# Kernel optimization log

Measured on AMD Instinct MI355X. Metric: run time of the kernel, lower is better.

## Reference

```python
import jax, jax.numpy as jnp
import numpy as np
import math

B, S, D_MODEL, N_HEAD, D_HEAD, D_FFN = 1, 2048, 1024, 16, 64, 4096
EPS = 1e-6


def setup_inputs() -> dict:
    key = jax.random.key(0)
    ks = jax.random.split(key, 10)
    scale = 0.02
    x = jax.random.normal(ks[0], (B, S, D_MODEL), dtype=jnp.float32)
    # RoPE frequencies: freqs_cis[s, i] = exp(1j * s * theta_i), theta_i = 10000^{-2i/d_head}
    half = D_HEAD // 2
    inv_freq = 1.0 / (10000.0 ** (jnp.arange(0, half, dtype=jnp.float32) * 2.0 / D_HEAD))
    angles = jnp.arange(S, dtype=jnp.float32)[:, None] * inv_freq[None, :]  # [S, half]
    freqs_cos = jnp.cos(angles)
    freqs_sin = jnp.sin(angles)
    wq = jax.random.normal(ks[1], (D_MODEL, N_HEAD * D_HEAD), dtype=jnp.float32) * scale
    wk = jax.random.normal(ks[2], (D_MODEL, N_HEAD * D_HEAD), dtype=jnp.float32) * scale
    wv = jax.random.normal(ks[3], (D_MODEL, N_HEAD * D_HEAD), dtype=jnp.float32) * scale
    wo = jax.random.normal(ks[4], (N_HEAD * D_HEAD, D_MODEL), dtype=jnp.float32) * scale
    w1 = jax.random.normal(ks[5], (D_MODEL, D_FFN), dtype=jnp.float32) * scale
    w2 = jax.random.normal(ks[6], (D_FFN, D_MODEL), dtype=jnp.float32) * scale
    w3 = jax.random.normal(ks[7], (D_MODEL, D_FFN), dtype=jnp.float32) * scale
    attn_norm_w = jnp.ones((D_MODEL,), dtype=jnp.float32)
    ffn_norm_w = jnp.ones((D_MODEL,), dtype=jnp.float32)
    return {"x": x, "freqs_cos": freqs_cos, "freqs_sin": freqs_sin,
            "wq": wq, "wk": wk, "wv": wv, "wo": wo,
            "w1": w1, "w2": w2, "w3": w3,
            "attn_norm_w": attn_norm_w, "ffn_norm_w": ffn_norm_w}


def _rmsnorm(x, w):
    xf = x.astype(jnp.float32)
    inv = jax.lax.rsqrt(jnp.mean(xf * xf, axis=-1, keepdims=True) + EPS)
    return (xf * inv).astype(x.dtype) * w


def _rope(t, cos, sin):
    # t: [B, S, H, D]; treat last dim as interleaved (even, odd) complex pairs
    b, s, h, d = t.shape
    tr = t.astype(jnp.float32).reshape(b, s, h, d // 2, 2)
    te, to = tr[..., 0], tr[..., 1]
    c = cos[None, :, None, :]
    sn = sin[None, :, None, :]
    out = jnp.stack([te * c - to * sn, te * sn + to * c], axis=-1)
    return out.reshape(b, s, h, d).astype(t.dtype)


def reference(x, freqs_cos, freqs_sin, wq, wk, wv, wo, w1, w2, w3, attn_norm_w, ffn_norm_w):
    bsz, seqlen, _ = x.shape
    # --- attention sub-block ---
    hin = _rmsnorm(x, attn_norm_w)
    q = (hin @ wq).reshape(bsz, seqlen, N_HEAD, D_HEAD)
    k = (hin @ wk).reshape(bsz, seqlen, N_HEAD, D_HEAD)
    v = (hin @ wv).reshape(bsz, seqlen, N_HEAD, D_HEAD)
    q = _rope(q, freqs_cos, freqs_sin)
    k = _rope(k, freqs_cos, freqs_sin)
    # [B, H, S, S] scores, softmax in fp32 (no causal mask in original)
    scores = jnp.einsum('bqhd,bkhd->bhqk', q, k) / math.sqrt(D_HEAD)
    probs = jax.nn.softmax(scores.astype(jnp.float32), axis=-1).astype(q.dtype)
    attn = jnp.einsum('bhqk,bkhd->bqhd', probs, v).reshape(bsz, seqlen, N_HEAD * D_HEAD)
    h = x + attn @ wo
    # --- SwiGLU FFN sub-block ---
    f = _rmsnorm(h, ffn_norm_w)
    ffn = (jax.nn.silu(f @ w1) * (f @ w3)) @ w2
    return h + ffn
```

## Files before the change

kernel.cpp:

```cpp
#include <hip/hip_runtime.h>
#include <stdint.h>
#include <stddef.h>

using bf16x8 = __attribute__((ext_vector_type(8))) __bf16;
using f32x4  = __attribute__((ext_vector_type(4))) float;

__device__ __forceinline__ float bf2f(unsigned short u) {
  union { unsigned int i; float f; } v; v.i = ((unsigned int)u) << 16; return v.f;
}
__device__ __forceinline__ unsigned short f2bf(float f) {
  union { float f; unsigned int i; } v; v.f = f;
  unsigned int r = v.i + 0x7fffu + ((v.i >> 16) & 1u);
  return (unsigned short)(r >> 16);
}
__device__ __forceinline__ unsigned short f2bf_trunc(float f) {
  union { float f; unsigned int i; } v; v.f = f;
  return (unsigned short)(v.i >> 16);
}
__device__ __forceinline__ void async16(const void* g, void* l) {
  __builtin_amdgcn_global_load_lds(
      (const __attribute__((address_space(1))) unsigned int*)g,
      (__attribute__((address_space(3))) unsigned int*)l, 16, 0, 0);
}

#define S_LEN 2048
#define DMODEL 1024
#define NHEAD 16
#define DHEAD 64
#define DFFN 4096

struct T4 {
  const float *s0, *s1, *s2, *s3;
  unsigned short *d0, *d1, *d2, *d3;
};
__global__ __launch_bounds__(256) void transpose4_k(T4 j) {
  const float* in = blockIdx.z == 0 ? j.s0 : blockIdx.z == 1 ? j.s1 : blockIdx.z == 2 ? j.s2 : j.s3;
  unsigned short* out = blockIdx.z == 0 ? j.d0 : blockIdx.z == 1 ? j.d1 : blockIdx.z == 2 ? j.d2 : j.d3;
  __shared__ unsigned short tile[32][33];
  const int tx = threadIdx.x & 31;
  const int ty = threadIdx.x >> 5;
  const int bc = blockIdx.x * 32;
  const int br = blockIdx.y * 32;
#pragma unroll
  for (int i = 0; i < 4; ++i)
    tile[ty + i * 8][tx] = f2bf(in[(size_t)(br + ty + i * 8) * 1024 + bc + tx]);
  __syncthreads();
#pragma unroll
  for (int i = 0; i < 4; ++i)
    out[(size_t)(bc + ty + i * 8) * 1024 + br + tx] = tile[tx][ty + i * 8];
}

__global__ __launch_bounds__(256) void transpose13_k(
    const float* __restrict__ w1, const float* __restrict__ w3,
    unsigned short* __restrict__ out) {
  const float* in = blockIdx.z ? w3 : w1;
  const int rb = blockIdx.z * 16;
  __shared__ unsigned short tile[32][33];
  const int tx = threadIdx.x & 31;
  const int ty = threadIdx.x >> 5;
  const int bc = blockIdx.x * 32;
  const int br = blockIdx.y * 32;
#pragma unroll
  for (int i = 0; i < 4; ++i)
    tile[ty + i * 8][tx] = f2bf(in[(size_t)(br + ty + i * 8) * 4096 + bc + tx]);
  __syncthreads();
#pragma unroll
  for (int i = 0; i < 4; ++i) {
    int c = bc + ty + i * 8;
    int dest = (c >> 4) * 32 + rb + (c & 15);
    out[(size_t)dest * 1024 + br + tx] = tile[tx][ty + i * 8];
  }
}

__global__ __launch_bounds__(256) void transpose_w2_k(
    const float* __restrict__ in, unsigned short* __restrict__ out) {
  __shared__ unsigned short tile[32][33];
  const int tx = threadIdx.x & 31;
  const int ty = threadIdx.x >> 5;
  const int bc = blockIdx.x * 32;
  const int br = blockIdx.y * 32;
#pragma unroll
  for (int i = 0; i < 4; ++i)
    tile[ty + i * 8][tx] = f2bf(in[(size_t)(br + ty + i * 8) * 1024 + bc + tx]);
  __syncthreads();
#pragma unroll
  for (int i = 0; i < 4; ++i)
    out[(size_t)(bc + ty + i * 8) * 4096 + br + tx] = tile[tx][ty + i * 8];
}

__global__ __launch_bounds__(256) void vtrans_k(
    const unsigned short* __restrict__ QKV, unsigned short* __restrict__ VtG) {
  __shared__ unsigned short tile[32][33];
  const int tx = threadIdx.x & 31;
  const int ty = threadIdx.x >> 5;
  const int bc = blockIdx.x * 32;
  const int br = blockIdx.y * 32;
#pragma unroll
  for (int i = 0; i < 4; ++i)
    tile[ty + i * 8][tx] = QKV[(size_t)(br + ty + i * 8) * 3072 + 2048 + bc + tx];
  __syncthreads();
#pragma unroll
  for (int i = 0; i < 4; ++i)
    VtG[(size_t)(bc + ty + i * 8) * 2048 + br + tx] = tile[tx][ty + i * 8];
}

__global__ __launch_bounds__(256) void rmsnorm_k(
    const float* __restrict__ X, const float* __restrict__ W,
    unsigned short* __restrict__ Y) {
  const int row = blockIdx.x;
  const int t = threadIdx.x;
  const int lane = t & 63, w = t >> 6;
  const float* x = X + (size_t)row * DMODEL;
  float xs[4];
  float s = 0.f;
#pragma unroll
  for (int i = 0; i < 4; ++i) {
    xs[i] = x[t * 4 + i];
    s += xs[i] * xs[i];
  }
#pragma unroll
  for (int m = 1; m < 64; m <<= 1) s += __shfl_xor(s, m, 64);
  __shared__ float red[4];
  if (lane == 0) red[w] = s;
  __syncthreads();
  float tot = red[0] + red[1] + red[2] + red[3];
  float inv = rsqrtf(tot * (1.0f / DMODEL) + 1e-6f);
#pragma unroll
  for (int i = 0; i < 4; ++i)
    Y[(size_t)row * DMODEL + t * 4 + i] = f2bf(xs[i] * inv * W[t * 4 + i]);
}

template <int MODE>
__global__ __launch_bounds__(256) void gemm_bt(
    const unsigned short* __restrict__ A, int lda,
    const unsigned short* __restrict__ BT,
    void* __restrict__ Cout,
    int K, int N) {
  __shared__ unsigned short As[128 * 32];
  __shared__ unsigned short Bs[128 * 32];
  const int t = threadIdx.x;
  const int lane = t & 63;
  const int w = t >> 6;
  const int qr = (w >> 1) * 64, qc = (w & 1) * 64;
  const int row16 = lane & 15, quad = lane >> 4;
  const int m0 = blockIdx.y * 128, n0 = blockIdx.x * 128;

  f32x4 acc[4][4] = {};

  for (int k0 = 0; k0 < K; k0 += 32) {
    __syncthreads();
#pragma unroll
    for (int p = 0; p < 2; ++p) {
      int off = p * 2048 + t * 8;
      int r = off >> 5, c = off & 31;
      async16(A + (size_t)(m0 + r) * lda + (k0 + c), &As[off]);
      async16(BT + (size_t)(n0 + r) * K + (k0 + c), &Bs[off]);
    }
    __syncthreads();
    bf16x8 a[4], b[4];
#pragma unroll
    for (int i = 0; i < 4; ++i) {
      a[i] = *(const bf16x8*)&As[(qr + i * 16 + row16) * 32 + quad * 8];
      b[i] = *(const bf16x8*)&Bs[(qc + i * 16 + row16) * 32 + quad * 8];
    }
#pragma unroll
    for (int i = 0; i < 4; ++i)
#pragma unroll
      for (int j = 0; j < 4; ++j)
        acc[i][j] = __builtin_amdgcn_mfma_f32_16x16x32_bf16(a[i], b[j], acc[i][j], 0, 0, 0);
  }

  if constexpr (MODE == 2) {
    unsigned short* C = (unsigned short*)Cout;
    const int ld = N >> 1;
#pragma unroll
    for (int i = 0; i < 4; ++i)
#pragma unroll
      for (int jp = 0; jp < 4; jp += 2)
#pragma unroll
        for (int reg = 0; reg < 4; ++reg) {
          int rr = m0 + qr + i * 16 + quad * 4 + reg;
          int cc = (n0 >> 1) + (qc >> 1) + (jp >> 1) * 16 + row16;
          float a1 = acc[i][jp][reg];
          float a3 = acc[i][jp + 1][reg];
          float f = a1 / (1.f + __expf(-a1)) * a3;
          C[(size_t)rr * ld + cc] = f2bf(f);
        }
  } else {
    unsigned short* C = (unsigned short*)Cout;
#pragma unroll
    for (int i = 0; i < 4; ++i)
#pragma unroll
      for (int j = 0; j < 4; ++j)
#pragma unroll
        for (int reg = 0; reg < 4; ++reg) {
          int rr = m0 + qr + i * 16 + quad * 4 + reg;
          int cc = n0 + qc + j * 16 + row16;
          C[(size_t)rr * N + cc] = f2bf(acc[i][j][reg]);
        }
  }
}

struct PtrPair { float* p0; float* p1; };

__global__ __launch_bounds__(256) void gemm_bt_sk(
    const unsigned short* __restrict__ A, int lda,
    const unsigned short* __restrict__ BT,
    PtrPair parts, int Kc, int Ktot, int N) {
  __shared__ unsigned short As[64 * 32];
  __shared__ unsigned short Bs[128 * 32];
  const int t = threadIdx.x;
  const int lane = t & 63;
  const int w = t >> 6;
  const int qr = (w >> 1) * 32, qc = (w & 1) * 64;
  const int row16 = lane & 15, quad = lane >> 4;
  const int m0 = blockIdx.y * 64, n0 = blockIdx.x * 128;
  const int kb = blockIdx.z * Kc;

  f32x4 acc[2][4] = {};

  for (int k0 = 0; k0 < Kc; k0 += 32) {
    __syncthreads();
    {
      int off = t * 8;
      int r = off >> 5, c = off & 31;
      async16(A + (size_t)(m0 + r) * lda + (kb + k0 + c), &As[off]);
    }
#pragma unroll
    for (int p = 0; p < 2; ++p) {
      int off = p * 2048 + t * 8;
      int r = off >> 5, c = off & 31;
      async16(BT + (size_t)(n0 + r) * Ktot + (kb + k0 + c), &Bs[off]);
    }
    __syncthreads();
    bf16x8 a[2], b[4];
#pragma unroll
    for (int i = 0; i < 2; ++i)
      a[i] = *(const bf16x8*)&As[(qr + i * 16 + row16) * 32 + quad * 8];
#pragma unroll
    for (int j = 0; j < 4; ++j)
      b[j] = *(const bf16x8*)&Bs[(qc + j * 16 + row16) * 32 + quad * 8];
#pragma unroll
    for (int i = 0; i < 2; ++i)
#pragma unroll
      for (int j = 0; j < 4; ++j)
        acc[i][j] = __builtin_amdgcn_mfma_f32_16x16x32_bf16(a[i], b[j], acc[i][j], 0, 0, 0);
  }

  float* C = blockIdx.z ? parts.p1 : parts.p0;
#pragma unroll
  for (int i = 0; i < 2; ++i)
#pragma unroll
    for (int j = 0; j < 4; ++j)
#pragma unroll
      for (int reg = 0; reg < 4; ++reg) {
        int rr = m0 + qr + i * 16 + quad * 4 + reg;
        int cc = n0 + qc + j * 16 + row16;
        C[(size_t)rr * N + cc] = acc[i][j][reg];
      }
}

__global__ __launch_bounds__(256) void reduce2_k(
    const float4* __restrict__ P0, const float4* __restrict__ P1,
    const float4* __restrict__ R, float4* __restrict__ Out, int nvec) {
  int i = blockIdx.x * 256 + threadIdx.x;
  if (i >= nvec) return;
  float4 a = P0[i], b = P1[i], r = R[i];
  float4 o;
  o.x = a.x + b.x + r.x;
  o.y = a.y + b.y + r.y;
  o.z = a.z + b.z + r.z;
  o.w = a.w + b.w + r.w;
  Out[i] = o;
}

__global__ __launch_bounds__(256) void rope_k(
    unsigned short* __restrict__ QKV,
    const float* __restrict__ cosp,
    const float* __restrict__ sinp) {
  int idx = blockIdx.x * 256 + threadIdx.x;
  int s = idx >> 9;
  int rem = idx & 511;
  int h = rem >> 5;
  int i = rem & 31;
  float c = cosp[s * 32 + i];
  float sn = sinp[s * 32 + i];
  size_t off = (size_t)s * 3072 + h * 64 + 2 * i;
  {
    float e = bf2f(QKV[off]), o = bf2f(QKV[off + 1]);
    QKV[off] = f2bf(e * c - o * sn);
    QKV[off + 1] = f2bf(e * sn + o * c);
  }
  {
    float e = bf2f(QKV[off + 1024]), o = bf2f(QKV[off + 1025]);
    QKV[off + 1024] = f2bf((e * c - o * sn) * 0.125f);
    QKV[off + 1025] = f2bf((e * sn + o * c) * 0.125f);
  }
}

#define VPAD 132
__device__ __forceinline__ int swz(int row, int col) { return col ^ ((row & 7) * 8); }

__global__ __launch_bounds__(256) void attn_k(
    const unsigned short* __restrict__ QKV,
    const unsigned short* __restrict__ VtG,
    float* __restrict__ O0, float* __restrict__ O1,
    float* __restrict__ L) {
  const int h = blockIdx.y;
  const int qb = blockIdx.x;
  const int z = blockIdx.z;
  const int t = threadIdx.x;
  const int lane = t & 63;
  const int w = t >> 6;
  const int row16 = lane & 15, quad = lane >> 4;
  const int q0 = qb * 64 + w * 16;
  const int kbase = z * 1024;

  __shared__ unsigned short Ks[128 * 64];
  __shared__ unsigned short Vt[64 * 128];
  __shared__ unsigned short Ps[4][16 * VPAD];

  const unsigned short* Qp = QKV;
  const unsigned short* Kp = QKV + 1024;
  const unsigned short* Vg = VtG + (size_t)h * 64 * 2048;

  bf16x8 aq[2];
#pragma unroll
  for (int kk = 0; kk < 2; ++kk)
    aq[kk] = *(const bf16x8*)(Qp + (size_t)(q0 + row16) * 3072 + h * 64 + kk * 32 + quad * 8);

  f32x4 o[4] = {};
  float l_r[4] = {0.f, 0.f, 0.f, 0.f};

  bf16x8 kreg[4], vreg[4];
#pragma unroll
  for (int p = 0; p < 4; ++p) {
    int off = p * 2048 + t * 8;
    int r = off >> 6, c = off & 63;
    kreg[p] = *(const bf16x8*)(Kp + (size_t)(kbase + r) * 3072 + h * 64 + c);
    int d = off >> 7, key = off & 127;
    vreg[p] = *(const bf16x8*)(Vg + (size_t)d * 2048 + kbase + key);
  }

  for (int kb = kbase; kb < kbase + 1024; kb += 128) {
    __syncthreads();
#pragma unroll
    for (int p = 0; p < 4; ++p) {
      int off = p * 2048 + t * 8;
      int r = off >> 6, c = off & 63;
      *(bf16x8*)&Ks[r * 64 + swz(r, c)] = kreg[p];
      int d = off >> 7, key = off & 127;
      *(bf16x8*)&Vt[d * 128 + swz(d, key)] = vreg[p];
    }
    __syncthreads();
    if (kb + 128 < kbase + 1024) {
      int kb2 = kb + 128;
#pragma unroll
      for (int p = 0; p < 4; ++p) {
        int off = p * 2048 + t * 8;
        int r = off >> 6, c = off & 63;
        kreg[p] = *(const bf16x8*)(Kp + (size_t)(kb2 + r) * 3072 + h * 64 + c);
        int d = off >> 7, key = off & 127;
        vreg[p] = *(const bf16x8*)(Vg + (size_t)d * 2048 + kb2 + key);
      }
    }

    f32x4 sc[8];
#pragma unroll
    for (int tj = 0; tj < 8; ++tj) {
      int kr = tj * 16 + row16;
      bf16x8 b0 = *(const bf16x8*)&Ks[kr * 64 + swz(kr, quad * 8)];
      bf16x8 b1 = *(const bf16x8*)&Ks[kr * 64 + swz(kr, 32 + quad * 8)];
      f32x4 z4 = {};
      z4 = __builtin_amdgcn_mfma_f32_16x16x32_bf16(aq[0], b0, z4, 0, 0, 0);
      z4 = __builtin_amdgcn_mfma_f32_16x16x32_bf16(aq[1], b1, z4, 0, 0, 0);
      sc[tj] = z4;
    }

#pragma unroll
    for (int reg = 0; reg < 4; ++reg) {
      float ssum = 0.f;
#pragma unroll
      for (int tj = 0; tj < 8; ++tj) {
        float p = __expf(sc[tj][reg]);
        sc[tj][reg] = p;
        ssum += p;
      }
#pragma unroll
      for (int m = 1; m < 16; m <<= 1) ssum += __shfl_xor(ssum, m, 16);
      l_r[reg] += ssum;
    }

#pragma unroll
    for (int tj = 0; tj < 8; ++tj)
#pragma unroll
      for (int reg = 0; reg < 4; ++reg)
        Ps[w][(quad * 4 + reg) * VPAD + tj * 16 + row16] = f2bf_trunc(sc[tj][reg]);

    bf16x8 ap[4];
#pragma unroll
    for (int kk = 0; kk < 4; ++kk)
      ap[kk] = *(const bf16x8*)&Ps[w][row16 * VPAD + kk * 32 + quad * 8];
#pragma unroll
    for (int dt = 0; dt < 4; ++dt) {
      int dr = dt * 16 + row16;
#pragma unroll
      for (int kk = 0; kk < 4; ++kk) {
        bf16x8 bv = *(const bf16x8*)&Vt[dr * 128 + swz(dr, kk * 32 + quad * 8)];
        o[dt] = __builtin_amdgcn_mfma_f32_16x16x32_bf16(ap[kk], bv, o[dt], 0, 0, 0);
      }
    }
  }

  float* Op = z ? O1 : O0;
#pragma unroll
  for (int dt = 0; dt < 4; ++dt)
#pragma unroll
    for (int reg = 0; reg < 4; ++reg)
      Op[(size_t)(q0 + quad * 4 + reg) * DMODEL + h * 64 + dt * 16 + row16] = o[dt][reg];
  if (row16 == 0)
#pragma unroll
    for (int reg = 0; reg < 4; ++reg)
      L[(size_t)(h * 2 + z) * S_LEN + q0 + quad * 4 + reg] = l_r[reg];
}

__global__ __launch_bounds__(256) void attn_combine_k(
    const float4* __restrict__ O0, const float4* __restrict__ O1,
    const float* __restrict__ L, unsigned short* __restrict__ Attn) {
  int i = blockIdx.x * 256 + threadIdx.x;
  int e0 = i * 4;
  int s = e0 >> 10;
  int c = e0 & 1023;
  int h = c >> 6;
  float la = L[(size_t)(h * 2) * S_LEN + s];
  float lb = L[(size_t)(h * 2 + 1) * S_LEN + s];
  float inv = 1.f / (la + lb);
  float4 a = O0[i], b = O1[i];
  ushort4 r;
  r.x = f2bf((a.x + b.x) * inv);
  r.y = f2bf((a.y + b.y) * inv);
  r.z = f2bf((a.z + b.z) * inv);
  r.w = f2bf((a.w + b.w) * inv);
  *(ushort4*)(Attn + e0) = r;
}

extern "C" void kernel_launch(void* const* d_in, const int* in_sizes, int n_in,
                              void* d_out, int out_size, void* d_ws, size_t ws_size,
                              hipStream_t stream) {
  (void)in_sizes; (void)n_in; (void)out_size; (void)ws_size;
  const float* x    = (const float*)d_in[0];
  const float* fcos = (const float*)d_in[1];
  const float* fsin = (const float*)d_in[2];
  const float* wq   = (const float*)d_in[3];
  const float* wk   = (const float*)d_in[4];
  const float* wv   = (const float*)d_in[5];
  const float* wo   = (const float*)d_in[6];
  const float* w1   = (const float*)d_in[7];
  const float* w2   = (const float*)d_in[8];
  const float* w3   = (const float*)d_in[9];
  const float* anw  = (const float*)d_in[10];
  const float* fnw  = (const float*)d_in[11];
  float* out = (float*)d_out;
  char* ws = (char*)d_ws;

  unsigned short* WqkvT = (unsigned short*)(ws + 0);
  unsigned short* VtG   = (unsigned short*)(ws + 0);
  float*          Lbuf  = (float*)(ws + 4194304);
  unsigned short* WoT   = (unsigned short*)(ws + 6291456);
  unsigned short* QKV   = (unsigned short*)(ws + 8388608);
  unsigned short* Attn  = (unsigned short*)(ws + 20971520);
  float* Oa             = (float*)(ws + 25165824);
  float* Ob             = (float*)(ws + 37748736);
  float* P0a            = (float*)(ws + 8388608);
  float* P1a            = (float*)(ws + 25165824);
  unsigned short* F     = (unsigned short*)(ws + 0);
  float* P0b            = (float*)(ws + 16777216);
  float* P1b            = (float*)(ws + 25165824);
  unsigned short* Hin   = (unsigned short*)(ws + 33554432);
  float*          Hres  = (float*)        (ws + 37748736);
  unsigned short* W13I  = (unsigned short*)(ws + 46137344);
  unsigned short* W2T   = (unsigned short*)(ws + 62914560);

  transpose4_k<<<dim3(32, 32, 4), 256, 0, stream>>>(
      T4{wq, wk, wv, wo, WqkvT, WqkvT + 1048576, WqkvT + 2097152, WoT});
  transpose13_k<<<dim3(128, 32, 2), 256, 0, stream>>>(w1, w3, W13I);
  transpose_w2_k<<<dim3(32, 128), 256, 0, stream>>>(w2, W2T);

  rmsnorm_k<<<2048, 256, 0, stream>>>(x, anw, Hin);
  gemm_bt<0><<<dim3(24, 16), 256, 0, stream>>>(Hin, 1024, WqkvT, QKV, 1024, 3072);
  rope_k<<<4096, 256, 0, stream>>>(QKV, fcos, fsin);
  vtrans_k<<<dim3(32, 64), 256, 0, stream>>>(QKV, VtG);
  attn_k<<<dim3(32, 16, 2), 256, 0, stream>>>(QKV, VtG, Oa, Ob, Lbuf);
  attn_combine_k<<<2048, 256, 0, stream>>>((const float4*)Oa, (const float4*)Ob, Lbuf, Attn);
  gemm_bt_sk<<<dim3(8, 32, 2), 256, 0, stream>>>(Attn, 1024, WoT, PtrPair{P0a, P1a}, 512, 1024, 1024);
  reduce2_k<<<2048, 256, 0, stream>>>((const float4*)P0a, (const float4*)P1a,
                                      (const float4*)x, (float4*)Hres, 524288);

  rmsnorm_k<<<2048, 256, 0, stream>>>(Hres, fnw, Hin);
  gemm_bt<2><<<dim3(64, 16), 256, 0, stream>>>(Hin, 1024, W13I, F, 1024, 8192);
  gemm_bt_sk<<<dim3(8, 32, 2), 256, 0, stream>>>(F, 4096, W2T, PtrPair{P0b, P1b}, 2048, 4096, 1024);
  reduce2_k<<<2048, 256, 0, stream>>>((const float4*)P0b, (const float4*)P1b,
                                      (const float4*)Hres, (float4*)out, 524288);
}
```

Before: 343.0 us.

## Switch GEMMs to 32x32x16 MFMA with K=64 tiles and XOR-swizzled LDS

Both GEMM kernels move from 16x16x32 to 32x32x16 bf16 MFMA instructions and double the K step per LDS stage to 64. LDS rows are XOR-swizzled in 16-byte chunks to avoid bank conflicts on the wider rows. The w1/w3 interleave in the transpose is widened from 16 to 32 columns so the fused SwiGLU epilogue can pair accumulators from the new tile shape. The aim is fewer LDS reads and barriers per FLOP and better MFMA throughput. In exchange, LDS use per block doubles, which may lower occupancy.

New measurement: 313.8 us. 8.5% less time.

```diff
diff --git a/kernel.cpp b/kernel.cpp
--- a/kernel.cpp
+++ b/kernel.cpp
@@ -4,6 +4,7 @@
 
 using bf16x8 = __attribute__((ext_vector_type(8))) __bf16;
 using f32x4  = __attribute__((ext_vector_type(4))) float;
+using f32x16 = __attribute__((ext_vector_type(16))) float;
 
 __device__ __forceinline__ float bf2f(unsigned short u) {
   union { unsigned int i; float f; } v; v.i = ((unsigned int)u) << 16; return v.f;
@@ -54,7 +55,7 @@
     const float* __restrict__ w1, const float* __restrict__ w3,
     unsigned short* __restrict__ out) {
   const float* in = blockIdx.z ? w3 : w1;
-  const int rb = blockIdx.z * 16;
+  const int rb = blockIdx.z * 32;
   __shared__ unsigned short tile[32][33];
   const int tx = threadIdx.x & 31;
   const int ty = threadIdx.x >> 5;
@@ -67,7 +68,7 @@
 #pragma unroll
   for (int i = 0; i < 4; ++i) {
     int c = bc + ty + i * 8;
-    int dest = (c >> 4) * 32 + rb + (c & 15);
+    int dest = (c >> 5) * 64 + rb + (c & 31);
     out[(size_t)dest * 1024 + br + tx] = tile[tx][ty + i * 8];
   }
 }
@@ -136,67 +137,74 @@
     const unsigned short* __restrict__ BT,
     void* __restrict__ Cout,
     int K, int N) {
-  __shared__ unsigned short As[128 * 32];
-  __shared__ unsigned short Bs[128 * 32];
+  __shared__ unsigned short As[128 * 64];
+  __shared__ unsigned short Bs[128 * 64];
   const int t = threadIdx.x;
   const int lane = t & 63;
   const int w = t >> 6;
   const int qr = (w >> 1) * 64, qc = (w & 1) * 64;
-  const int row16 = lane & 15, quad = lane >> 4;
+  const int l31 = lane & 31, half = lane >> 5;
   const int m0 = blockIdx.y * 128, n0 = blockIdx.x * 128;
 
-  f32x4 acc[4][4] = {};
-
-  for (int k0 = 0; k0 < K; k0 += 32) {
+  f32x16 acc[2][2] = {};
+
+  int srow[4], scol[4];
+#pragma unroll
+  for (int p = 0; p < 4; ++p) {
+    int off = p * 2048 + t * 8;
+    int r = off >> 6;
+    srow[p] = r;
+    scol[p] = (((off >> 3) & 7) ^ (r & 7)) * 8;
+  }
+
+  for (int k0 = 0; k0 < K; k0 += 64) {
     __syncthreads();
 #pragma unroll
-    for (int p = 0; p < 2; ++p) {
+    for (int p = 0; p < 4; ++p) {
       int off = p * 2048 + t * 8;
-      int r = off >> 5, c = off & 31;
-      async16(A + (size_t)(m0 + r) * lda + (k0 + c), &As[off]);
-      async16(BT + (size_t)(n0 + r) * K + (k0 + c), &Bs[off]);
+      async16(A + (size_t)(m0 + srow[p]) * lda + (k0 + scol[p]), &As[off]);
+      async16(BT + (size_t)(n0 + srow[p]) * K + (k0 + scol[p]), &Bs[off]);
     }
     __syncthreads();
-    bf16x8 a[4], b[4];
-#pragma unroll
-    for (int i = 0; i < 4; ++i) {
-      a[i] = *(const bf16x8*)&As[(qr + i * 16 + row16) * 32 + quad * 8];
-      b[i] = *(const bf16x8*)&Bs[(qc + i * 16 + row16) * 32 + quad * 8];
-    }
-#pragma unroll
-    for (int i = 0; i < 4; ++i)
-#pragma unroll
-      for (int j = 0; j < 4; ++j)
-        acc[i][j] = __builtin_amdgcn_mfma_f32_16x16x32_bf16(a[i], b[j], acc[i][j], 0, 0, 0);
+#pragma unroll
+    for (int ks = 0; ks < 4; ++ks) {
+      const int ch = ((ks * 2 + half) ^ (l31 & 7)) * 8;
+      bf16x8 a0 = *(const bf16x8*)&As[(qr + l31) * 64 + ch];
+      bf16x8 a1 = *(const bf16x8*)&As[(qr + 32 + l31) * 64 + ch];
+      bf16x8 b0 = *(const bf16x8*)&Bs[(qc + l31) * 64 + ch];
+      bf16x8 b1 = *(const bf16x8*)&Bs[(qc + 32 + l31) * 64 + ch];
+      acc[0][0] = __builtin_amdgcn_mfma_f32_32x32x16_bf16(a0, b0, acc[0][0], 0, 0, 0);
+      acc[0][1] = __builtin_amdgcn_mfma_f32_32x32x16_bf16(a0, b1, acc[0][1], 0, 0, 0);
+      acc[1][0] = __builtin_amdgcn_mfma_f32_32x32x16_bf16(a1, b0, acc[1][0], 0, 0, 0);
+      acc[1][1] = __builtin_amdgcn_mfma_f32_32x32x16_bf16(a1, b1, acc[1][1], 0, 0, 0);
+    }
   }
 
   if constexpr (MODE == 2) {
     unsigned short* C = (unsigned short*)Cout;
     const int ld = N >> 1;
 #pragma unroll
-    for (int i = 0; i < 4; ++i)
-#pragma unroll
-      for (int jp = 0; jp < 4; jp += 2)
-#pragma unroll
-        for (int reg = 0; reg < 4; ++reg) {
-          int rr = m0 + qr + i * 16 + quad * 4 + reg;
-          int cc = (n0 >> 1) + (qc >> 1) + (jp >> 1) * 16 + row16;
-          float a1 = acc[i][jp][reg];
-          float a3 = acc[i][jp + 1][reg];
-          float f = a1 / (1.f + __expf(-a1)) * a3;
-          C[(size_t)rr * ld + cc] = f2bf(f);
-        }
+    for (int rt = 0; rt < 2; ++rt)
+#pragma unroll
+      for (int reg = 0; reg < 16; ++reg) {
+        int rr = m0 + qr + rt * 32 + (reg & 3) + 8 * (reg >> 2) + 4 * half;
+        int cc = ((n0 + qc) >> 1) + l31;
+        float a1v = acc[rt][0][reg];
+        float a3v = acc[rt][1][reg];
+        float f = a1v / (1.f + __expf(-a1v)) * a3v;
+        C[(size_t)rr * ld + cc] = f2bf(f);
+      }
   } else {
     unsigned short* C = (unsigned short*)Cout;
 #pragma unroll
-    for (int i = 0; i < 4; ++i)
-#pragma unroll
-      for (int j = 0; j < 4; ++j)
-#pragma unroll
-        for (int reg = 0; reg < 4; ++reg) {
-          int rr = m0 + qr + i * 16 + quad * 4 + reg;
-          int cc = n0 + qc + j * 16 + row16;
-          C[(size_t)rr * N + cc] = f2bf(acc[i][j][reg]);
+    for (int rt = 0; rt < 2; ++rt)
+#pragma unroll
+      for (int ct = 0; ct < 2; ++ct)
+#pragma unroll
+        for (int reg = 0; reg < 16; ++reg) {
+          int rr = m0 + qr + rt * 32 + (reg & 3) + 8 * (reg >> 2) + 4 * half;
+          int cc = n0 + qc + ct * 32 + l31;
+          C[(size_t)rr * N + cc] = f2bf(acc[rt][ct][reg]);
         }
   }
 }
@@ -207,57 +215,55 @@
     const unsigned short* __restrict__ A, int lda,
     const unsigned short* __restrict__ BT,
     PtrPair parts, int Kc, int Ktot, int N) {
-  __shared__ unsigned short As[64 * 32];
-  __shared__ unsigned short Bs[128 * 32];
+  __shared__ unsigned short As[64 * 64];
+  __shared__ unsigned short Bs[128 * 64];
   const int t = threadIdx.x;
   const int lane = t & 63;
   const int w = t >> 6;
   const int qr = (w >> 1) * 32, qc = (w & 1) * 64;
-  const int row16 = lane & 15, quad = lane >> 4;
+  const int l31 = lane & 31, half = lane >> 5;
   const int m0 = blockIdx.y * 64, n0 = blockIdx.x * 128;
   const int kb = blockIdx.z * Kc;
 
-  f32x4 acc[2][4] = {};
-
-  for (int k0 = 0; k0 < Kc; k0 += 32) {
+  f32x16 acc[2] = {};
+
+  for (int k0 = 0; k0 < Kc; k0 += 64) {
     __syncthreads();
-    {
-      int off = t * 8;
-      int r = off >> 5, c = off & 31;
-      async16(A + (size_t)(m0 + r) * lda + (kb + k0 + c), &As[off]);
-    }
 #pragma unroll
     for (int p = 0; p < 2; ++p) {
       int off = p * 2048 + t * 8;
-      int r = off >> 5, c = off & 31;
-      async16(BT + (size_t)(n0 + r) * Ktot + (kb + k0 + c), &Bs[off]);
+      int r = off >> 6;
+      int sc = (((off >> 3) & 7) ^ (r & 7)) * 8;
+      async16(A + (size_t)(m0 + r) * lda + (kb + k0 + sc), &As[off]);
+    }
+#pragma unroll
+    for (int p = 0; p < 4; ++p) {
+      int off = p * 2048 + t * 8;
+      int r = off >> 6;
+      int sc = (((off >> 3) & 7) ^ (r & 7)) * 8;
+      async16(BT + (size_t)(n0 + r) * Ktot + (kb + k0 + sc), &Bs[off]);
     }
     __syncthreads();
-    bf16x8 a[2], b[4];
-#pragma unroll
-    for (int i = 0; i < 2; ++i)
-      a[i] = *(const bf16x8*)&As[(qr + i * 16 + row16) * 32 + quad * 8];
-#pragma unroll
-    for (int j = 0; j < 4; ++j)
-      b[j] = *(const bf16x8*)&Bs[(qc + j * 16 + row16) * 32 + quad * 8];
-#pragma unroll
-    for (int i = 0; i < 2; ++i)
-#pragma unroll
-      for (int j = 0; j < 4; ++j)
-        acc[i][j] = __builtin_amdgcn_mfma_f32_16x16x32_bf16(a[i], b[j], acc[i][j], 0, 0, 0);
+#pragma unroll
+    for (int ks = 0; ks < 4; ++ks) {
+      const int ch = ((ks * 2 + half) ^ (l31 & 7)) * 8;
+      bf16x8 a0 = *(const bf16x8*)&As[(qr + l31) * 64 + ch];
+      bf16x8 b0 = *(const bf16x8*)&Bs[(qc + l31) * 64 + ch];
+      bf16x8 b1 = *(const bf16x8*)&Bs[(qc + 32 + l31) * 64 + ch];
+      acc[0] = __builtin_amdgcn_mfma_f32_32x32x16_bf16(a0, b0, acc[0], 0, 0, 0);
+      acc[1] = __builtin_amdgcn_mfma_f32_32x32x16_bf16(a0, b1, acc[1], 0, 0, 0);
+    }
   }
 
   float* C = blockIdx.z ? parts.p1 : parts.p0;
 #pragma unroll
-  for (int i = 0; i < 2; ++i)
-#pragma unroll
-    for (int j = 0; j < 4; ++j)
-#pragma unroll
-      for (int reg = 0; reg < 4; ++reg) {
-        int rr = m0 + qr + i * 16 + quad * 4 + reg;
-        int cc = n0 + qc + j * 16 + row16;
-        C[(size_t)rr * N + cc] = acc[i][j][reg];
-      }
+  for (int ct = 0; ct < 2; ++ct)
+#pragma unroll
+    for (int reg = 0; reg < 16; ++reg) {
+      int rr = m0 + qr + (reg & 3) + 8 * (reg >> 2) + 4 * half;
+      int cc = n0 + qc + ct * 32 + l31;
+      C[(size_t)rr * N + cc] = acc[ct][reg];
+    }
 }
 
 __global__ __launch_bounds__(256) void reduce2_k(
```
